# Kernel optimization log

Hardware: AMD Instinct MI355X
Metric: run time of the kernel (lower is better)

Reference implementation:

```python
import jax, jax.numpy as jnp
import numpy as np

B, I, M, D, H = 2, 2048, 2048, 1024, 16
Dh = D // H


def setup_inputs() -> dict:
    key = jax.random.key(0)
    ks = jax.random.split(key, 7)
    s = 0.02
    return {
        "input_BxIxDi": jax.random.normal(ks[0], (B, I, D), jnp.float32),
        "memory_BxMxDi": jax.random.normal(ks[1], (B, M, D), jnp.float32),
        "bias_BxIxM": jnp.zeros((B, I, M), jnp.float32),
        "Wq": jax.random.normal(ks[2], (D, D), jnp.float32) * s,
        "Wk": jax.random.normal(ks[3], (D, D), jnp.float32) * s,
        "Wv": jax.random.normal(ks[4], (D, D), jnp.float32) * s,
        "Wo": jax.random.normal(ks[5], (D, D), jnp.float32) * s,
    }


def _split_heads(x_bid):  # [B, L, D] -> [B, H, L, Dh]
    b, l, _ = x_bid.shape
    return x_bid.reshape(b, l, H, Dh).transpose(0, 2, 1, 3)


def reference(input_BxIxDi, memory_BxMxDi, bias_BxIxM, Wq, Wk, Wv, Wo):
    q = _split_heads(input_BxIxDi @ Wq) * (Dh ** -0.5)  # [B,H,I,Dh]
    k = _split_heads(memory_BxMxDi @ Wk)                # [B,H,M,Dh]
    v = _split_heads(memory_BxMxDi @ Wv)                # [B,H,M,Dh]
    logits = jnp.einsum("bhid,bhmd->bhim", q, k) + bias_BxIxM[:, None, :, :]
    align = jax.nn.softmax(logits, axis=-1)             # [B,H,I,M]
    out = jnp.einsum("bhim,bhmd->bhid", align, v)       # [B,H,I,Dh]
    out = out.transpose(0, 2, 1, 3).reshape(out.shape[0], out.shape[2], D)
    out = out @ Wo                                      # [B,I,D]
    return out, align
```

## Files before the change

### kernel.cpp

```cpp
#include <hip/hip_runtime.h>

#define B_ 2
#define I_ 2048
#define M_ 2048
#define D_ 1024
#define H_ 16
#define Dh_ 64
#define SWZ(r, c) ((c) ^ (((r) & 7) << 2))

typedef __bf16 bf16_t;
typedef __bf16 bf16x8 __attribute__((ext_vector_type(8)));
typedef __bf16 bf16x4 __attribute__((ext_vector_type(4)));
typedef float f32x4 __attribute__((ext_vector_type(4)));

__device__ __forceinline__ bf16_t f2b(float f) {
    union { float f; unsigned u; } in;
    in.f = f;
    unsigned r = (in.u + 0x7fffu + ((in.u >> 16) & 1u)) >> 16;
    union { unsigned short s; bf16_t b; } out;
    out.s = (unsigned short)r;
    return out.b;
}

__device__ __forceinline__ unsigned cvt_pk_bf16(float lo, float hi) {
    unsigned r;
    asm("v_cvt_pk_bf16_f32 %0, %1, %2" : "=v"(r) : "v"(lo), "v"(hi));
    return r;
}

__global__ void cast_f32_bf16(const float* __restrict__ src, bf16_t* __restrict__ dst, int n) {
    int idx = (blockIdx.x * blockDim.x + threadIdx.x) * 4;
    if (idx + 3 < n) {
        float4 v = *(const float4*)(src + idx);
        bf16x4 o;
        o[0] = f2b(v.x); o[1] = f2b(v.y); o[2] = f2b(v.z); o[3] = f2b(v.w);
        *(bf16x4*)(dst + idx) = o;
    }
}

__global__ void transpose_cast(const float* __restrict__ src, bf16_t* __restrict__ dst) {
    __shared__ float tile[32][33];
    int n0 = blockIdx.x * 32, k0 = blockIdx.y * 32;
    int tx = threadIdx.x, ty = threadIdx.y;
#pragma unroll
    for (int i = 0; i < 4; i++)
        tile[ty + i * 8][tx] = src[(size_t)(k0 + ty + i * 8) * D_ + n0 + tx];
    __syncthreads();
#pragma unroll
    for (int i = 0; i < 4; i++)
        dst[(size_t)(n0 + ty + i * 8) * D_ + k0 + tx] = f2b(tile[tx][ty + i * 8]);
}

template <int MODE>
__global__ __launch_bounds__(256) void gemm_nt(const bf16_t* __restrict__ A,
                                               const bf16_t* __restrict__ Bt,
                                               void* __restrict__ Cout, float scale) {
    constexpr int LDT = 40;
    __shared__ bf16_t As[128 * LDT];
    __shared__ bf16_t Bs[128 * LDT];
    int m0 = blockIdx.x * 128, n0 = blockIdx.y * 128;
    int tid = threadIdx.x;
    int wave = tid >> 6, lane = tid & 63, quad = lane >> 4, l16 = lane & 15;
    int wr = wave >> 1, wc = wave & 1;
    f32x4 acc[4][4] = {};

    for (int k0 = 0; k0 < D_; k0 += 32) {
#pragma unroll
        for (int c = tid; c < 512; c += 256) {
            int r = c >> 2, ko = (c & 3) * 8;
            *(bf16x8*)&As[r * LDT + ko] = *(const bf16x8*)&A[(size_t)(m0 + r) * D_ + k0 + ko];
            *(bf16x8*)&Bs[r * LDT + ko] = *(const bf16x8*)&Bt[(size_t)(n0 + r) * D_ + k0 + ko];
        }
        __syncthreads();
        bf16x8 af[4], bfr[4];
#pragma unroll
        for (int i = 0; i < 4; i++) af[i] = *(bf16x8*)&As[(wr * 64 + i * 16 + l16) * LDT + quad * 8];
#pragma unroll
        for (int j = 0; j < 4; j++) bfr[j] = *(bf16x8*)&Bs[(wc * 64 + j * 16 + l16) * LDT + quad * 8];
#pragma unroll
        for (int i = 0; i < 4; i++)
#pragma unroll
            for (int j = 0; j < 4; j++)
                acc[i][j] = __builtin_amdgcn_mfma_f32_16x16x32_bf16(af[i], bfr[j], acc[i][j], 0, 0, 0);
        __syncthreads();
    }

    if (MODE == 1) {
        bf16_t* Ts = As;
#pragma unroll
        for (int s = 0; s < 4; s++) {
            __syncthreads();
            if (wc == (s >> 1)) {
#pragma unroll
                for (int jj = 0; jj < 2; jj++) {
                    int j = (s & 1) * 2 + jj;
#pragma unroll
                    for (int i = 0; i < 4; i++)
#pragma unroll
                        for (int r = 0; r < 4; r++)
                            Ts[(jj * 16 + l16) * 136 + wr * 64 + i * 16 + quad * 4 + r] =
                                f2b(acc[i][j][r] * scale);
                }
            }
            __syncthreads();
#pragma unroll
            for (int it = 0; it < 2; it++) {
                int task = it * 256 + tid;
                int ns = task >> 4, ch = task & 15;
                int n = n0 + s * 32 + ns;
                int m = m0 + ch * 8;
                int bb = m >> 11, mm = m & 2047, hh = n >> 6, d = n & 63;
                *(bf16x8*)&((bf16_t*)Cout)[(((size_t)(bb * H_ + hh) * Dh_ + d) << 11) + mm] =
                    *(bf16x8*)&Ts[ns * 136 + ch * 8];
            }
        }
        return;
    }

#pragma unroll
    for (int i = 0; i < 4; i++)
#pragma unroll
        for (int j = 0; j < 4; j++) {
            int n = n0 + wc * 64 + j * 16 + l16;
#pragma unroll
            for (int r = 0; r < 4; r++) {
                int m = m0 + wr * 64 + i * 16 + quad * 4 + r;
                float v = acc[i][j][r] * scale;
                if (MODE == 0) {
                    ((bf16_t*)Cout)[(size_t)m * D_ + n] = f2b(v);
                } else {
                    ((float*)Cout)[(size_t)m * D_ + n] = v;
                }
            }
        }
}

__global__ __launch_bounds__(1024) void attn_fused(const bf16_t* __restrict__ Q,
                                                   const bf16_t* __restrict__ K,
                                                   const bf16_t* __restrict__ Vt,
                                                   const float* __restrict__ bias,
                                                   float* __restrict__ align_out,
                                                   bf16_t* __restrict__ AO) {
    extern __shared__ float S[];
    __shared__ float rowinv[16];
    int i0 = blockIdx.x * 16, h = blockIdx.y, b = blockIdx.z;
    int tid = threadIdx.x, wave = tid >> 6, lane = tid & 63, quad = lane >> 4, l16 = lane & 15;

    size_t qrow = (size_t)(b * I_ + i0 + l16) * D_ + h * Dh_ + quad * 8;
    bf16x8 aq0 = *(const bf16x8*)&Q[qrow];
    bf16x8 aq1 = *(const bf16x8*)&Q[qrow + 32];

#pragma unroll
    for (int t = 0; t < 8; t++) {
        int m0 = wave * 128 + t * 16;
        size_t krow = (size_t)(b * M_ + m0 + l16) * D_ + h * Dh_ + quad * 8;
        bf16x8 bk0 = *(const bf16x8*)&K[krow];
        bf16x8 bk1 = *(const bf16x8*)&K[krow + 32];
        f32x4 acc = {};
        acc = __builtin_amdgcn_mfma_f32_16x16x32_bf16(aq0, bk0, acc, 0, 0, 0);
        acc = __builtin_amdgcn_mfma_f32_16x16x32_bf16(aq1, bk1, acc, 0, 0, 0);
#pragma unroll
        for (int r = 0; r < 4; r++) {
            int i = quad * 4 + r;
            float v = acc[r] + bias[((size_t)b * I_ + i0 + i) * M_ + m0 + l16];
            S[i * 2048 + SWZ(i, m0 + l16)] = v;
        }
    }
    __syncthreads();

    {
        int row = wave;
        float* srow = &S[row * 2048];
        float mx = -1e30f;
#pragma unroll
        for (int t = 0; t < 8; t++) {
            float4 v = *(float4*)&srow[SWZ(row, lane * 4 + t * 256)];
            mx = fmaxf(mx, fmaxf(fmaxf(v.x, v.y), fmaxf(v.z, v.w)));
        }
#pragma unroll
        for (int off = 1; off < 64; off <<= 1) mx = fmaxf(mx, __shfl_xor(mx, off));
        float sum = 0.f;
#pragma unroll
        for (int t = 0; t < 8; t++) {
            float4 v = *(float4*)&srow[SWZ(row, lane * 4 + t * 256)];
            v.x = __expf(v.x - mx); v.y = __expf(v.y - mx);
            v.z = __expf(v.z - mx); v.w = __expf(v.w - mx);
            *(float4*)&srow[SWZ(row, lane * 4 + t * 256)] = v;
            sum += v.x + v.y + v.z + v.w;
        }
#pragma unroll
        for (int off = 1; off < 64; off <<= 1) sum += __shfl_xor(sum, off);
        if (lane == 0) rowinv[row] = 1.0f / sum;
    }
    __syncthreads();

    {
        float* dst = align_out + (((size_t)(b * H_ + h) * I_ + i0) << 11);
        for (int idx = tid; idx < 16 * 2048 / 4; idx += 1024) {
            int r = idx >> 9;
            int c = (idx & 511) * 4;
            float4 v = *(float4*)&S[r * 2048 + SWZ(r, c)];
            float iv = rowinv[r];
            v.x *= iv; v.y *= iv; v.z *= iv; v.w *= iv;
            *(float4*)&dst[((size_t)r << 11) + c] = v;
        }
    }

    {
        int cg = wave & 3, kg = wave >> 2;
        int n0 = cg * 16;
        f32x4 o0 = {}, o1 = {};
        const bf16_t* vrow = &Vt[((size_t)(b * H_ + h) * Dh_ + n0 + l16) << 11];
        const float* srow = &S[l16 * 2048];
#pragma unroll
        for (int t = 0; t < 8; t++) {
            int kt = kg * 512 + t * 64;
            int c0 = kt + quad * 8;
            float4 f0 = *(const float4*)&srow[SWZ(l16, c0)];
            float4 f1 = *(const float4*)&srow[SWZ(l16, c0 + 4)];
            float4 f2 = *(const float4*)&srow[SWZ(l16, c0 + 32)];
            float4 f3 = *(const float4*)&srow[SWZ(l16, c0 + 36)];
            union { bf16x8 v; unsigned u[4]; } a0, a1;
            a0.u[0] = cvt_pk_bf16(f0.x, f0.y); a0.u[1] = cvt_pk_bf16(f0.z, f0.w);
            a0.u[2] = cvt_pk_bf16(f1.x, f1.y); a0.u[3] = cvt_pk_bf16(f1.z, f1.w);
            a1.u[0] = cvt_pk_bf16(f2.x, f2.y); a1.u[1] = cvt_pk_bf16(f2.z, f2.w);
            a1.u[2] = cvt_pk_bf16(f3.x, f3.y); a1.u[3] = cvt_pk_bf16(f3.z, f3.w);
            bf16x8 v0 = *(const bf16x8*)&vrow[kt + quad * 8];
            bf16x8 v1 = *(const bf16x8*)&vrow[kt + 32 + quad * 8];
            o0 = __builtin_amdgcn_mfma_f32_16x16x32_bf16(a0.v, v0, o0, 0, 0, 0);
            o1 = __builtin_amdgcn_mfma_f32_16x16x32_bf16(a1.v, v1, o1, 0, 0, 0);
        }
        __syncthreads();
        float* scr = &S[(size_t)wave * 512 + (size_t)lane * 8];
        *(f32x4*)scr = o0;
        *(f32x4*)(scr + 4) = o1;
        __syncthreads();
        if (kg == 0) {
#pragma unroll
            for (int w2 = 1; w2 < 4; w2++) {
                const float* p = &S[(size_t)(w2 * 4 + cg) * 512 + (size_t)lane * 8];
                f32x4 p0 = *(const f32x4*)p;
                f32x4 p1 = *(const f32x4*)(p + 4);
                o0 += p0;
                o1 += p1;
            }
#pragma unroll
            for (int r = 0; r < 4; r++) {
                int i = quad * 4 + r;
                float v = (o0[r] + o1[r]) * rowinv[i];
                AO[(size_t)(b * I_ + i0 + i) * D_ + h * Dh_ + n0 + l16] = f2b(v);
            }
        }
    }
}

extern "C" void kernel_launch(void* const* d_in, const int* in_sizes, int n_in,
                              void* d_out, int out_size, void* d_ws, size_t ws_size,
                              hipStream_t stream) {
    const float* input  = (const float*)d_in[0];
    const float* memory = (const float*)d_in[1];
    const float* bias   = (const float*)d_in[2];
    const float* Wq     = (const float*)d_in[3];
    const float* Wk     = (const float*)d_in[4];
    const float* Wv     = (const float*)d_in[5];
    const float* Wo     = (const float*)d_in[6];

    float* out   = (float*)d_out;
    float* align = out + (size_t)B_ * I_ * D_;

    char* ws = (char*)d_ws;
    const size_t nBID = (size_t)B_ * I_ * D_;
    const size_t nDD  = (size_t)D_ * D_;
    bf16_t* in_b  = (bf16_t*)ws; ws += nBID * 2;
    bf16_t* mem_b = (bf16_t*)ws; ws += nBID * 2;
    bf16_t* Wq_t  = (bf16_t*)ws; ws += nDD * 2;
    bf16_t* Wk_t  = (bf16_t*)ws; ws += nDD * 2;
    bf16_t* Wv_t  = (bf16_t*)ws; ws += nDD * 2;
    bf16_t* Wo_t  = (bf16_t*)ws; ws += nDD * 2;
    bf16_t* Qb    = (bf16_t*)ws; ws += nBID * 2;
    bf16_t* Kb    = (bf16_t*)ws; ws += nBID * 2;
    bf16_t* Vt    = (bf16_t*)ws; ws += nBID * 2;
    bf16_t* AO    = (bf16_t*)ws; ws += nBID * 2;

    cast_f32_bf16<<<nBID / 1024, 256, 0, stream>>>(input, in_b, (int)nBID);
    cast_f32_bf16<<<nBID / 1024, 256, 0, stream>>>(memory, mem_b, (int)nBID);
    dim3 tb(32, 8), tg(32, 32);
    transpose_cast<<<tg, tb, 0, stream>>>(Wq, Wq_t);
    transpose_cast<<<tg, tb, 0, stream>>>(Wk, Wk_t);
    transpose_cast<<<tg, tb, 0, stream>>>(Wv, Wv_t);
    transpose_cast<<<tg, tb, 0, stream>>>(Wo, Wo_t);

    dim3 gg(32, 8);
    gemm_nt<0><<<gg, 256, 0, stream>>>(in_b, Wq_t, Qb, 0.125f);
    gemm_nt<0><<<gg, 256, 0, stream>>>(mem_b, Wk_t, Kb, 1.0f);
    gemm_nt<1><<<gg, 256, 0, stream>>>(mem_b, Wv_t, Vt, 1.0f);

    attn_fused<<<dim3(I_ / 16, H_, B_), 1024, 16 * 2048 * 4, stream>>>(Qb, Kb, Vt, bias, align, AO);

    gemm_nt<2><<<gg, 256, 0, stream>>>(AO, Wo_t, out, 1.0f);
}
```

Before: 1.109 ms.

## Retile GEMMs to 64x64 with direct global-to-LDS loads, merge prep kernels, remap attention grid

```diff
diff --git a/kernel.cpp b/kernel.cpp
--- a/kernel.cpp
+++ b/kernel.cpp
@@ -28,7 +28,15 @@
     return r;
 }
 
-__global__ void cast_f32_bf16(const float* __restrict__ src, bf16_t* __restrict__ dst, int n) {
+__device__ __forceinline__ void gload_lds16(const bf16_t* g, bf16_t* l) {
+    __builtin_amdgcn_global_load_lds((const __attribute__((address_space(1))) void*)g,
+                                     (__attribute__((address_space(3))) void*)l, 16, 0, 0);
+}
+
+__global__ void cast_f32_bf16_2(const float* __restrict__ a, bf16_t* __restrict__ da,
+                                const float* __restrict__ b, bf16_t* __restrict__ db, int n) {
+    const float* src = blockIdx.z ? b : a;
+    bf16_t* dst = blockIdx.z ? db : da;
     int idx = (blockIdx.x * blockDim.x + threadIdx.x) * 4;
     if (idx + 3 < n) {
         float4 v = *(const float4*)(src + idx);
@@ -38,7 +46,12 @@
     }
 }
 
-__global__ void transpose_cast(const float* __restrict__ src, bf16_t* __restrict__ dst) {
+__global__ void transpose_cast4(const float* __restrict__ s0, const float* __restrict__ s1,
+                                const float* __restrict__ s2, const float* __restrict__ s3,
+                                bf16_t* __restrict__ d0, bf16_t* __restrict__ d1,
+                                bf16_t* __restrict__ d2, bf16_t* __restrict__ d3) {
+    const float* src = blockIdx.z == 0 ? s0 : blockIdx.z == 1 ? s1 : blockIdx.z == 2 ? s2 : s3;
+    bf16_t* dst = blockIdx.z == 0 ? d0 : blockIdx.z == 1 ? d1 : blockIdx.z == 2 ? d2 : d3;
     __shared__ float tile[32][33];
     int n0 = blockIdx.x * 32, k0 = blockIdx.y * 32;
     int tx = threadIdx.x, ty = threadIdx.y;
@@ -52,79 +65,81 @@
 }
 
 template <int MODE>
-__global__ __launch_bounds__(256) void gemm_nt(const bf16_t* __restrict__ A,
-                                               const bf16_t* __restrict__ Bt,
-                                               void* __restrict__ Cout, float scale) {
-    constexpr int LDT = 40;
-    __shared__ bf16_t As[128 * LDT];
-    __shared__ bf16_t Bs[128 * LDT];
-    int m0 = blockIdx.x * 128, n0 = blockIdx.y * 128;
+__global__ __launch_bounds__(256, 4) void gemm_nt(const bf16_t* __restrict__ A,
+                                                  const bf16_t* __restrict__ Bt,
+                                                  void* __restrict__ Cout, float scale) {
+    __shared__ __align__(16) bf16_t As[64 * 64];
+    __shared__ __align__(16) bf16_t Bs[64 * 64];
+    int m0 = blockIdx.x * 64, n0 = blockIdx.y * 64;
     int tid = threadIdx.x;
     int wave = tid >> 6, lane = tid & 63, quad = lane >> 4, l16 = lane & 15;
     int wr = wave >> 1, wc = wave & 1;
-    f32x4 acc[4][4] = {};
-
-    for (int k0 = 0; k0 < D_; k0 += 32) {
-#pragma unroll
-        for (int c = tid; c < 512; c += 256) {
-            int r = c >> 2, ko = (c & 3) * 8;
-            *(bf16x8*)&As[r * LDT + ko] = *(const bf16x8*)&A[(size_t)(m0 + r) * D_ + k0 + ko];
-            *(bf16x8*)&Bs[r * LDT + ko] = *(const bf16x8*)&Bt[(size_t)(n0 + r) * D_ + k0 + ko];
-        }
-        __syncthreads();
-        bf16x8 af[4], bfr[4];
-#pragma unroll
-        for (int i = 0; i < 4; i++) af[i] = *(bf16x8*)&As[(wr * 64 + i * 16 + l16) * LDT + quad * 8];
-#pragma unroll
-        for (int j = 0; j < 4; j++) bfr[j] = *(bf16x8*)&Bs[(wc * 64 + j * 16 + l16) * LDT + quad * 8];
-#pragma unroll
-        for (int i = 0; i < 4; i++)
-#pragma unroll
-            for (int j = 0; j < 4; j++)
-                acc[i][j] = __builtin_amdgcn_mfma_f32_16x16x32_bf16(af[i], bfr[j], acc[i][j], 0, 0, 0);
+    f32x4 acc[2][2] = {};
+
+    int srow = tid >> 3, schunk = tid & 7;
+    int sw = schunk ^ (srow & 7);
+    const bf16_t* ga = &A[(size_t)(m0 + srow) * D_ + sw * 8];
+    const bf16_t* gb = &Bt[(size_t)(n0 + srow) * D_ + sw * 8];
+    bf16_t* la = &As[tid * 8];
+    bf16_t* lb = &Bs[tid * 8];
+
+    for (int k0 = 0; k0 < D_; k0 += 64) {
+        gload_lds16(ga + k0, la);
+        gload_lds16(ga + k0 + 32 * D_, la + 2048);
+        gload_lds16(gb + k0, lb);
+        gload_lds16(gb + k0 + 32 * D_, lb + 2048);
+        __syncthreads();
+        bf16x8 af[2][2], bfr[2][2];
+#pragma unroll
+        for (int t = 0; t < 2; t++)
+#pragma unroll
+            for (int ks = 0; ks < 2; ks++) {
+                int ca = ((ks * 4 + quad) ^ (l16 & 7)) * 8;
+                af[t][ks] = *(bf16x8*)&As[(wr * 32 + t * 16 + l16) * 64 + ca];
+                bfr[t][ks] = *(bf16x8*)&Bs[(wc * 32 + t * 16 + l16) * 64 + ca];
+            }
+#pragma unroll
+        for (int i = 0; i < 2; i++)
+#pragma unroll
+            for (int j = 0; j < 2; j++)
+#pragma unroll
+                for (int ks = 0; ks < 2; ks++)
+                    acc[i][j] = __builtin_amdgcn_mfma_f32_16x16x32_bf16(af[i][ks], bfr[j][ks],
+                                                                        acc[i][j], 0, 0, 0);
         __syncthreads();
     }
 
     if (MODE == 1) {
         bf16_t* Ts = As;
 #pragma unroll
-        for (int s = 0; s < 4; s++) {
-            __syncthreads();
-            if (wc == (s >> 1)) {
-#pragma unroll
-                for (int jj = 0; jj < 2; jj++) {
-                    int j = (s & 1) * 2 + jj;
-#pragma unroll
-                    for (int i = 0; i < 4; i++)
-#pragma unroll
-                        for (int r = 0; r < 4; r++)
-                            Ts[(jj * 16 + l16) * 136 + wr * 64 + i * 16 + quad * 4 + r] =
-                                f2b(acc[i][j][r] * scale);
+        for (int j = 0; j < 2; j++)
+#pragma unroll
+            for (int i = 0; i < 2; i++)
+#pragma unroll
+                for (int rp = 0; rp < 2; rp++) {
+                    unsigned pk = cvt_pk_bf16(acc[i][j][rp * 2] * scale, acc[i][j][rp * 2 + 1] * scale);
+                    *(unsigned*)&Ts[(wc * 32 + j * 16 + l16) * 64 + wr * 32 + i * 16 + quad * 4 + rp * 2] = pk;
                 }
-            }
-            __syncthreads();
-#pragma unroll
-            for (int it = 0; it < 2; it++) {
-                int task = it * 256 + tid;
-                int ns = task >> 4, ch = task & 15;
-                int n = n0 + s * 32 + ns;
-                int m = m0 + ch * 8;
-                int bb = m >> 11, mm = m & 2047, hh = n >> 6, d = n & 63;
-                *(bf16x8*)&((bf16_t*)Cout)[(((size_t)(bb * H_ + hh) * Dh_ + d) << 11) + mm] =
-                    *(bf16x8*)&Ts[ns * 136 + ch * 8];
-            }
+        __syncthreads();
+        int bb = m0 >> 11, hh = n0 >> 6, mmb = m0 & 2047;
+        bf16_t* dst = (bf16_t*)Cout + (((size_t)(bb * H_ + hh) * Dh_) << 11) + mmb;
+#pragma unroll
+        for (int it = 0; it < 2; it++) {
+            int task = it * 256 + tid;
+            int d = task >> 3, ch = task & 7;
+            *(bf16x8*)&dst[((size_t)d << 11) + ch * 8] = *(bf16x8*)&Ts[d * 64 + ch * 8];
         }
         return;
     }
 
 #pragma unroll
-    for (int i = 0; i < 4; i++)
-#pragma unroll
-        for (int j = 0; j < 4; j++) {
-            int n = n0 + wc * 64 + j * 16 + l16;
+    for (int i = 0; i < 2; i++)
+#pragma unroll
+        for (int j = 0; j < 2; j++) {
+            int n = n0 + wc * 32 + j * 16 + l16;
 #pragma unroll
             for (int r = 0; r < 4; r++) {
-                int m = m0 + wr * 64 + i * 16 + quad * 4 + r;
+                int m = m0 + wr * 32 + i * 16 + quad * 4 + r;
                 float v = acc[i][j][r] * scale;
                 if (MODE == 0) {
                     ((bf16_t*)Cout)[(size_t)m * D_ + n] = f2b(v);
@@ -143,7 +158,11 @@
                                                    bf16_t* __restrict__ AO) {
     extern __shared__ float S[];
     __shared__ float rowinv[16];
-    int i0 = blockIdx.x * 16, h = blockIdx.y, b = blockIdx.z;
+    int p = blockIdx.x;
+    int L = (p & 7) * 512 + (p >> 3);
+    int i0 = (L & 127) * 16;
+    int h = (L >> 7) & 15;
+    int b = L >> 11;
     int tid = threadIdx.x, wave = tid >> 6, lane = tid & 63, quad = lane >> 4, l16 = lane & 15;
 
     size_t qrow = (size_t)(b * I_ + i0 + l16) * D_ + h * Dh_ + quad * 8;
@@ -238,9 +257,9 @@
         if (kg == 0) {
 #pragma unroll
             for (int w2 = 1; w2 < 4; w2++) {
-                const float* p = &S[(size_t)(w2 * 4 + cg) * 512 + (size_t)lane * 8];
-                f32x4 p0 = *(const f32x4*)p;
-                f32x4 p1 = *(const f32x4*)(p + 4);
+                const float* pp = &S[(size_t)(w2 * 4 + cg) * 512 + (size_t)lane * 8];
+                f32x4 p0 = *(const f32x4*)pp;
+                f32x4 p1 = *(const f32x4*)(pp + 4);
                 o0 += p0;
                 o1 += p1;
             }
@@ -282,20 +301,15 @@
     bf16_t* Vt    = (bf16_t*)ws; ws += nBID * 2;
     bf16_t* AO    = (bf16_t*)ws; ws += nBID * 2;
 
-    cast_f32_bf16<<<nBID / 1024, 256, 0, stream>>>(input, in_b, (int)nBID);
-    cast_f32_bf16<<<nBID / 1024, 256, 0, stream>>>(memory, mem_b, (int)nBID);
-    dim3 tb(32, 8), tg(32, 32);
-    transpose_cast<<<tg, tb, 0, stream>>>(Wq, Wq_t);
-    transpose_cast<<<tg, tb, 0, stream>>>(Wk, Wk_t);
-    transpose_cast<<<tg, tb, 0, stream>>>(Wv, Wv_t);
-    transpose_cast<<<tg, tb, 0, stream>>>(Wo, Wo_t);
-
-    dim3 gg(32, 8);
+    cast_f32_bf16_2<<<dim3(nBID / 1024, 1, 2), 256, 0, stream>>>(input, in_b, memory, mem_b, (int)nBID);
+    transpose_cast4<<<dim3(32, 32, 4), dim3(32, 8), 0, stream>>>(Wq, Wk, Wv, Wo, Wq_t, Wk_t, Wv_t, Wo_t);
+
+    dim3 gg(64, 16);
     gemm_nt<0><<<gg, 256, 0, stream>>>(in_b, Wq_t, Qb, 0.125f);
     gemm_nt<0><<<gg, 256, 0, stream>>>(mem_b, Wk_t, Kb, 1.0f);
     gemm_nt<1><<<gg, 256, 0, stream>>>(mem_b, Wv_t, Vt, 1.0f);
 
-    attn_fused<<<dim3(I_ / 16, H_, B_), 1024, 16 * 2048 * 4, stream>>>(Qb, Kb, Vt, bias, align, AO);
+    attn_fused<<<dim3(4096), 1024, 16 * 2048 * 4, stream>>>(Qb, Kb, Vt, bias, align, AO);
 
     gemm_nt<2><<<gg, 256, 0, stream>>>(AO, Wo_t, out, 1.0f);
 }
```

Measured after the change: 1.036 ms. 6.6% less time.
